# Kernel optimization log

Measured on AMD Instinct MI355X. Metric: run time of the kernel, lower is better.

Reference implementation:

```python
import jax, jax.numpy as jnp
import numpy as np
import math

B, N, DIM, H, DH, NNULL = 2, 2048, 1024, 16, 64, 2
SCALE = 8.0
LN_EPS = 1e-5


def _alibi_slopes(heads):
    # heads is a power of 2 here (16): slopes = start * start**i
    start = 2.0 ** (-(2.0 ** (-(math.log2(heads) - 3))))
    return np.array([start * (start ** i) for i in range(heads)], dtype=np.float32)


def setup_inputs() -> dict:
    key = jax.random.key(0)
    ks = jax.random.split(key, 6)
    inner = H * DH
    return {
        "x": jax.random.normal(ks[0], (B, N, DIM), dtype=jnp.float32),
        "norm_g": jnp.ones((DIM,), jnp.float32),
        "norm_b": jnp.zeros((DIM,), jnp.float32),
        "Wq": jax.random.normal(ks[1], (DIM, inner), jnp.float32) * 0.02,
        "Wkv": jax.random.normal(ks[2], (DIM, 2 * inner), jnp.float32) * 0.02,
        "q_scale": jnp.ones((DH,), jnp.float32),
        "k_scale": jnp.ones((DH,), jnp.float32),
        "null_kv": jax.random.normal(ks[3], (H, 2 * NNULL, DH), jnp.float32),
        "Wout": jax.random.normal(ks[4], (inner, DIM), jnp.float32) * 0.02,
    }


def _l2norm(t):
    # matches F.normalize: x / max(||x||, 1e-12)
    n = jnp.sqrt(jnp.sum(t * t, axis=-1, keepdims=True))
    return t / jnp.maximum(n, 1e-12)


def reference(x, norm_g, norm_b, Wq, Wkv, q_scale, k_scale, null_kv, Wout):
    b, n, dim = x.shape
    h, dh, nn = H, DH, NNULL
    j = n + nn

    # NOTE: faithful to source -- K/V come from the PRE-norm x (kv_input bound
    # before x = self.norm(x)); only Q uses the LayerNorm'd x.
    mu = jnp.mean(x, axis=-1, keepdims=True)
    var = jnp.mean((x - mu) ** 2, axis=-1, keepdims=True)
    xn = (x - mu) * jax.lax.rsqrt(var + LN_EPS) * norm_g + norm_b

    q = (xn @ Wq).reshape(b, n, h, dh).transpose(0, 2, 1, 3)          # b h n d
    kv = x @ Wkv
    k, v = jnp.split(kv, 2, axis=-1)
    k = k.reshape(b, n, h, dh).transpose(0, 2, 1, 3)                   # b h n d
    v = v.reshape(b, n, h, dh).transpose(0, 2, 1, 3)

    # null kv: (h, 2*nn, dh) -> (h, nn, 2, dh)
    null = null_kv.reshape(h, nn, 2, dh)
    nk = jnp.broadcast_to(null[:, :, 0, :][None], (b, h, nn, dh))
    nv = jnp.broadcast_to(null[:, :, 1, :][None], (b, h, nn, dh))
    k = jnp.concatenate([nk, k], axis=2)                               # b h j d
    v = jnp.concatenate([nv, v], axis=2)

    q = _l2norm(q) * q_scale
    k = _l2norm(k) * k_scale

    sim = jnp.einsum('bhid,bhjd->bhij', q, k) * SCALE                  # b h n j

    # ALiBi bias: rows at positions j-n..j-1, cols 0..j-1
    irow = jnp.arange(j - n, j)
    jcol = jnp.arange(j)
    bias = -jnp.abs(jcol[None, :] - irow[:, None]).astype(sim.dtype)   # (n, j)
    slopes = jnp.asarray(_alibi_slopes(h))[:, None, None]              # (h,1,1)
    sim = sim + slopes * bias

    # causal mask: triu with offset j - n + 1 (null kv always visible)
    causal = jnp.triu(jnp.ones((n, j), dtype=bool), k=j - n + 1)
    neg = jnp.finfo(sim.dtype).max
    sim = jnp.where(causal[None, None], -neg, sim)

    attn = jax.nn.softmax(sim, axis=-1)
    out = jnp.einsum('bhij,bhjd->bhid', attn, v)
    out = out.transpose(0, 2, 1, 3).reshape(b, n, h * dh)
    return out @ Wout
```

## Files before the change

kernel.cpp:

```cpp
#include <hip/hip_runtime.h>
#include <stdint.h>

#define H_    16
#define N_    2048
#define DIM_  1024
#define DH_   64
#define NN_   2
#define J_    2050
#define JP_   2112
#define B_    2
#define M_    4096
#define NSEG_ 84

typedef unsigned short u16;
typedef unsigned int u32;
typedef short bf16x8 __attribute__((ext_vector_type(8)));
typedef float f32x4 __attribute__((ext_vector_type(4)));

__device__ __forceinline__ u16 f2b(float f) {
  union { float f; unsigned int i; } v; v.f = f;
  unsigned int r = v.i + 0x7fffu + ((v.i >> 16) & 1u);
  return (u16)(r >> 16);
}
__device__ __forceinline__ float b2f(u16 u) {
  union { unsigned int i; float f; } v; v.i = ((unsigned int)u) << 16; return v.f;
}
__device__ __forceinline__ float lo2f(u32 u) {
  union { u32 i; float f; } v; v.i = u << 16; return v.f;
}
__device__ __forceinline__ float hi2f(u32 u) {
  union { u32 i; float f; } v; v.i = u & 0xffff0000u; return v.f;
}
__device__ __forceinline__ void unp8(const uint4 u, float* d) {
  d[0] = lo2f(u.x); d[1] = hi2f(u.x); d[2] = lo2f(u.y); d[3] = hi2f(u.y);
  d[4] = lo2f(u.z); d[5] = hi2f(u.z); d[6] = lo2f(u.w); d[7] = hi2f(u.w);
}
__device__ __forceinline__ void dma16(const u16* g, u16* l) {
  __builtin_amdgcn_global_load_lds(
      (const __attribute__((address_space(1))) u32*)(const void*)g,
      (__attribute__((address_space(3))) u32*)(void*)l, 16, 0, 0);
}

__global__ __launch_bounds__(256) void ktranspose_cast(const float* __restrict__ in,
                                                       u16* __restrict__ out, int R, int C) {
  __shared__ float tile[32][33];
  int tx = threadIdx.x & 31, ty = threadIdx.x >> 5;
  int c0 = blockIdx.x * 32, r0 = blockIdx.y * 32;
  #pragma unroll
  for (int i = 0; i < 32; i += 8)
    tile[ty + i][tx] = in[(size_t)(r0 + ty + i) * C + c0 + tx];
  __syncthreads();
  #pragma unroll
  for (int i = 0; i < 32; i += 8)
    out[(size_t)(c0 + ty + i) * R + r0 + tx] = f2b(tile[tx][ty + i]);
}

__global__ __launch_bounds__(256) void lnorm_k(const float* __restrict__ x,
                                               const float* __restrict__ g,
                                               const float* __restrict__ bb,
                                               u16* __restrict__ xn,
                                               u16* __restrict__ xbf) {
  int row = blockIdx.x;
  int t = threadIdx.x;
  float4 rw = *(const float4*)(x + (size_t)row * DIM_ + t * 4);
  float v0 = rw.x, v1 = rw.y, v2 = rw.z, v3 = rw.w;
  uint2 cw;
  cw.x = (unsigned)f2b(v0) | ((unsigned)f2b(v1) << 16);
  cw.y = (unsigned)f2b(v2) | ((unsigned)f2b(v3) << 16);
  *(uint2*)(xbf + (size_t)row * DIM_ + t * 4) = cw;
  float s = v0 + v1 + v2 + v3;
  float ss = v0 * v0 + v1 * v1 + v2 * v2 + v3 * v3;
  #pragma unroll
  for (int o = 32; o; o >>= 1) { s += __shfl_xor(s, o, 64); ss += __shfl_xor(ss, o, 64); }
  __shared__ float red[8];
  int lane = t & 63, w = t >> 6;
  if (lane == 0) { red[w] = s; red[4 + w] = ss; }
  __syncthreads();
  float S = red[0] + red[1] + red[2] + red[3];
  float SS = red[4] + red[5] + red[6] + red[7];
  float mu = S * (1.0f / DIM_);
  float var = SS * (1.0f / DIM_) - mu * mu;
  float rs = rsqrtf(var + 1e-5f);
  float4 gv = *(const float4*)(g + t * 4);
  float4 bv = *(const float4*)(bb + t * 4);
  uint2 ow;
  ow.x = (unsigned)f2b((v0 - mu) * rs * gv.x + bv.x) |
         ((unsigned)f2b((v1 - mu) * rs * gv.y + bv.y) << 16);
  ow.y = (unsigned)f2b((v2 - mu) * rs * gv.z + bv.z) |
         ((unsigned)f2b((v3 - mu) * rs * gv.w + bv.w) << 16);
  *(uint2*)(xn + (size_t)row * DIM_ + t * 4) = ow;
}

template <int MODE>
__global__ __launch_bounds__(256, 4) void gemm_k(const u16* __restrict__ A,
                                                 const u16* __restrict__ BT,
                                                 void* __restrict__ dst0,
                                                 void* __restrict__ dst1,
                                                 const float* __restrict__ scale,
                                                 int M, int Nc, int K) {
  __shared__ u16 As[128 * 32];
  __shared__ u16 Bs[64 * 32];
  int tid = threadIdx.x, wv = tid >> 6, lane = tid & 63;
  int fm = lane & 15, fg = lane >> 4;
  int row0 = blockIdx.y * 128, col0 = blockIdx.x * 64;
  f32x4 acc[2][4] = {};
  int lr = lane >> 2, lc8 = (lane & 3) * 8;
  const u16* Ag = A + (size_t)(row0 + wv * 32 + lr) * K + lc8;
  const u16* Bg = BT + (size_t)(col0 + wv * 16 + lr) * K + lc8;
  u16* AsW = As + wv * 1024;
  u16* BsW = Bs + wv * 512;
  for (int k0 = 0; k0 < K; k0 += 32) {
    __syncthreads();
    dma16(Ag + k0, AsW);
    dma16(Ag + (size_t)16 * K + k0, AsW + 512);
    dma16(Bg + k0, BsW);
    __syncthreads();
    bf16x8 af0 = *(const bf16x8*)&As[(wv * 32 + fm) * 32 + fg * 8];
    bf16x8 af1 = *(const bf16x8*)&As[(wv * 32 + 16 + fm) * 32 + fg * 8];
    #pragma unroll
    for (int nt = 0; nt < 4; nt++) {
      bf16x8 bfr = *(const bf16x8*)&Bs[(nt * 16 + fm) * 32 + fg * 8];
      acc[0][nt] = __builtin_amdgcn_mfma_f32_16x16x32_bf16(af0, bfr, acc[0][nt], 0, 0, 0);
      acc[1][nt] = __builtin_amdgcn_mfma_f32_16x16x32_bf16(af1, bfr, acc[1][nt], 0, 0, 0);
    }
  }
  if (MODE == 1) {
    float* C = (float*)dst0;
    #pragma unroll
    for (int mt = 0; mt < 2; mt++)
      #pragma unroll
      for (int nt = 0; nt < 4; nt++)
        #pragma unroll
        for (int r = 0; r < 4; r++) {
          int m = row0 + wv * 32 + mt * 16 + fg * 4 + r;
          C[(size_t)m * Nc + col0 + nt * 16 + fm] = acc[mt][nt][r];
        }
  } else {
    bool isK = (MODE == 2) || (col0 < 1024);
    int h = ((MODE == 2) ? col0 : (isK ? col0 : col0 - 1024)) >> 6;
    float sv[4];
    if (isK) {
      #pragma unroll
      for (int nt = 0; nt < 4; nt++) sv[nt] = scale[nt * 16 + fm];
    }
    u16* Do = (u16*)((MODE == 3 && !isK) ? dst1 : dst0);
    #pragma unroll
    for (int mt = 0; mt < 2; mt++) {
      #pragma unroll
      for (int r = 0; r < 4; r++) {
        float inv = 1.0f;
        if (isK) {
          float ssp = 0.0f;
          #pragma unroll
          for (int nt = 0; nt < 4; nt++) ssp += acc[mt][nt][r] * acc[mt][nt][r];
          #pragma unroll
          for (int o = 1; o <= 8; o <<= 1) ssp += __shfl_xor(ssp, o, 64);
          inv = 1.0f / fmaxf(sqrtf(ssp), 1e-12f);
        }
        int m = row0 + wv * 32 + mt * 16 + fg * 4 + r;
        int b = m >> 11, n = m & 2047;
        size_t base;
        if (MODE == 2)      base = (((size_t)(b * H_ + h)) * N_ + n) * 64;
        else if (isK)       base = (((size_t)(b * H_ + h)) * JP_ + (n + NN_)) * 64;
        else                base = (((size_t)(b * H_ + h)) * J_ + (n + NN_)) * 64;
        #pragma unroll
        for (int nt = 0; nt < 4; nt++) {
          float val = acc[mt][nt][r];
          if (isK) val = val * inv * sv[nt];
          Do[base + nt * 16 + fm] = f2b(val);
        }
      }
    }
  }
}

__global__ __launch_bounds__(256) void vtransp_k(const u16* __restrict__ Vb,
                                                 const float* __restrict__ nkv,
                                                 const float* __restrict__ ks,
                                                 u16* __restrict__ Kb,
                                                 u16* __restrict__ VTp) {
  __shared__ u16 tile[64][80];
  int t = threadIdx.x;
  int c = blockIdx.x, bh = blockIdx.y, h = bh & 15;
  int jl = t >> 2, dc = (t & 3) * 16;
  int j = c * 64 + jl;
  if (j < NN_) {
    float kvv[16];
    float kssp = 0.0f;
    #pragma unroll
    for (int e = 0; e < 16; e++) {
      float vv = nkv[(size_t)(h * 4 + 2 * j + 1) * 64 + dc + e];
      tile[jl][dc + e] = f2b(vv);
      float kv = nkv[(size_t)(h * 4 + 2 * j) * 64 + dc + e];
      kvv[e] = kv; kssp += kv * kv;
    }
    kssp += __shfl_xor(kssp, 1, 64);
    kssp += __shfl_xor(kssp, 2, 64);
    float inv = 1.0f / fmaxf(sqrtf(kssp), 1e-12f);
    #pragma unroll
    for (int e = 0; e < 16; e++)
      Kb[((size_t)bh * JP_ + j) * 64 + dc + e] = f2b(kvv[e] * inv * ks[dc + e]);
  } else if (j < J_) {
    const uint4* src = (const uint4*)(Vb + ((size_t)bh * J_ + j) * 64 + dc);
    *(uint4*)&tile[jl][dc] = src[0];
    *(uint4*)&tile[jl][dc + 8] = src[1];
  } else {
    uint4 z = {0, 0, 0, 0};
    *(uint4*)&tile[jl][dc] = z;
    *(uint4*)&tile[jl][dc + 8] = z;
  }
  __syncthreads();
  int d = t >> 2, p0 = (t & 3) * 16;
  u16 tmp[16] __attribute__((aligned(16)));
  #pragma unroll
  for (int e = 0; e < 16; e++) {
    int pos = p0 + e;
    int h2 = pos >> 5, rem = pos & 31;
    int fgp = rem >> 3, tt = rem & 7;
    int nt = tt >> 2, r = tt & 3;
    int jloc = (h2 * 2 + nt) * 16 + fgp * 4 + r;
    tmp[e] = tile[jloc][d];
  }
  uint4* dstp = (uint4*)(VTp + ((size_t)bh * 64 + d) * JP_ + c * 64 + p0);
  dstp[0] = ((uint4*)tmp)[0];
  dstp[1] = ((uint4*)tmp)[1];
}

__global__ __launch_bounds__(256, 6) void attn_k(const u16* __restrict__ Qn,
                                                 const u16* __restrict__ Kb,
                                                 const u16* __restrict__ VTp,
                                                 const float* __restrict__ qs,
                                                 const float* __restrict__ ks,
                                                 u16* __restrict__ partials) {
  __shared__ u16 Ks0[64 * 32], Ks1[64 * 32];
  __shared__ u16 Vs0[64 * 32], Vs1[64 * 32];
  int tid = threadIdx.x;
  int wv = tid >> 6, lane = tid & 63;
  int fm = lane & 15, fg = lane >> 4;
  int bh = blockIdx.y, h = bh & 15;
  int cum = 0, qt = 0, seg = 0;
  #pragma unroll 1
  for (int i = 0; i < 32; i++) {
    int t = 31 - i, s = (t + 9) >> 3;
    if ((int)blockIdx.x < cum + s) { qt = t; seg = (int)blockIdx.x - cum; break; }
    cum += s;
  }
  int q0 = qt * 64;
  int q = q0 + wv * 16 + fm;
  float slope = exp2f(-0.5f * (float)(h + 1));
  float prod = fabsf(qs[lane] * ks[lane]);
  #pragma unroll
  for (int o = 32; o; o >>= 1) prod = fmaxf(prod, __shfl_xor(prod, o, 64));
  float Mb = 8.0f * prod;
  const u16* qp = Qn + ((size_t)bh * N_ + q) * 64 + fg * 8;
  bf16x8 qf0 = *(const bf16x8*)(qp);
  bf16x8 qf1 = *(const bf16x8*)(qp + 32);
  f32x4 accO[4] = {};
  float lp = 0.0f;
  int lr = lane >> 2, lc8 = (lane & 3) * 8;
  const u16* KbBH = Kb + (size_t)bh * JP_ * 64;
  const u16* VTbh = VTp + (size_t)bh * 64 * JP_;
  int c0 = seg * 8;
  int c1 = min(c0 + 8, qt + 2);
  for (int c = c0; c < c1; c++) {
    int jb = c * 64;
    __syncthreads();
    const u16* Kg = KbBH + (size_t)jb * 64 + (size_t)(wv * 16 + lr) * 64 + lc8;
    dma16(Kg,      Ks0 + wv * 512);
    dma16(Kg + 32, Ks1 + wv * 512);
    const u16* Vg = VTbh + (size_t)(wv * 16 + lr) * JP_ + jb + lc8;
    dma16(Vg,      Vs0 + wv * 512);
    dma16(Vg + 32, Vs1 + wv * 512);
    __syncthreads();
    f32x4 accS[4] = {};
    #pragma unroll
    for (int nt = 0; nt < 4; nt++) {
      bf16x8 kf0 = *(const bf16x8*)&Ks0[(nt * 16 + fm) * 32 + fg * 8];
      accS[nt] = __builtin_amdgcn_mfma_f32_16x16x32_bf16(kf0, qf0, accS[nt], 0, 0, 0);
      bf16x8 kf1 = *(const bf16x8*)&Ks1[(nt * 16 + fm) * 32 + fg * 8];
      accS[nt] = __builtin_amdgcn_mfma_f32_16x16x32_bf16(kf1, qf1, accS[nt], 0, 0, 0);
    }
    union { bf16x8 v; u16 s[8]; } P0, P1;
    #pragma unroll
    for (int nt = 0; nt < 4; nt++) {
      #pragma unroll
      for (int r = 0; r < 4; r++) {
        int jj = jb + nt * 16 + fg * 4 + r;
        float arg = fmaf(accS[nt][r], 8.0f, slope * (float)(jj - q - 2)) - Mb;
        float p = (jj <= q + 2) ? __expf(arg) : 0.0f;
        u16 pb = f2b(p);
        lp += b2f(pb);
        if (nt < 2) P0.s[nt * 4 + r] = pb;
        else        P1.s[(nt - 2) * 4 + r] = pb;
      }
    }
    #pragma unroll
    for (int nt = 0; nt < 4; nt++) {
      bf16x8 vf0 = *(const bf16x8*)&Vs0[(nt * 16 + fm) * 32 + fg * 8];
      accO[nt] = __builtin_amdgcn_mfma_f32_16x16x32_bf16(vf0, P0.v, accO[nt], 0, 0, 0);
      bf16x8 vf1 = *(const bf16x8*)&Vs1[(nt * 16 + fm) * 32 + fg * 8];
      accO[nt] = __builtin_amdgcn_mfma_f32_16x16x32_bf16(vf1, P1.v, accO[nt], 0, 0, 0);
    }
  }
  lp += __shfl_xor(lp, 16, 64);
  lp += __shfl_xor(lp, 32, 64);
  u16* P = partials + ((size_t)bh * NSEG_ + blockIdx.x) * 4224;
  int sq = wv * 16 + fm;
  #pragma unroll
  for (int nt = 0; nt < 4; nt++) {
    uint2 ow;
    ow.x = (unsigned)f2b(accO[nt][0]) | ((unsigned)f2b(accO[nt][1]) << 16);
    ow.y = (unsigned)f2b(accO[nt][2]) | ((unsigned)f2b(accO[nt][3]) << 16);
    *(uint2*)(P + sq * 64 + nt * 16 + fg * 4) = ow;
  }
  if (fg == 0) *(float*)(P + 4096 + 2 * sq) = lp;
}

__global__ __launch_bounds__(256) void comb_k(const u16* __restrict__ partials,
                                              u16* __restrict__ AO) {
  int qt = blockIdx.x, bh = blockIdx.y, b = bh >> 4, h = bh & 15;
  int t = threadIdx.x, q = t >> 2, dq = (t & 3) * 16;
  int s = (qt + 9) >> 3;
  int cum = 0;
  for (int tt = qt + 1; tt < 32; tt++) cum += (tt + 9) >> 3;
  float acc[16] = {};
  float lsum = 0.0f;
  for (int k = 0; k < s; k++) {
    const u16* P = partials + ((size_t)bh * NSEG_ + cum + k) * 4224;
    uint4 a = *(const uint4*)(P + q * 64 + dq);
    uint4 bq = *(const uint4*)(P + q * 64 + dq + 8);
    float tmp[8];
    unp8(a, tmp);
    #pragma unroll
    for (int e = 0; e < 8; e++) acc[e] += tmp[e];
    unp8(bq, tmp);
    #pragma unroll
    for (int e = 0; e < 8; e++) acc[8 + e] += tmp[e];
    lsum += *(const float*)(P + 4096 + 2 * q);
  }
  float linv = 1.0f / lsum;
  int n = qt * 64 + q;
  u16* dst = AO + (((size_t)(b * N_ + n)) * H_ + h) * 64 + dq;
  u16 ov[16] __attribute__((aligned(16)));
  #pragma unroll
  for (int e = 0; e < 16; e++) ov[e] = f2b(acc[e] * linv);
  *(uint4*)dst = ((uint4*)ov)[0];
  *(uint4*)(dst + 8) = ((uint4*)ov)[1];
}

extern "C" void kernel_launch(void* const* d_in, const int* in_sizes, int n_in,
                              void* d_out, int out_size, void* d_ws, size_t ws_size,
                              hipStream_t stream) {
  const float* x    = (const float*)d_in[0];
  const float* ng   = (const float*)d_in[1];
  const float* nb   = (const float*)d_in[2];
  const float* Wq   = (const float*)d_in[3];
  const float* Wkv  = (const float*)d_in[4];
  const float* qs   = (const float*)d_in[5];
  const float* ks   = (const float*)d_in[6];
  const float* nkv  = (const float*)d_in[7];
  const float* Wout = (const float*)d_in[8];
  float* out = (float*)d_out;
  char* ws = (char*)d_ws;

  u16* xn    = (u16*)(ws + 0);
  u16* WoutT = (u16*)(ws + 8388608);
  u16* Qn    = (u16*)(ws + 10485760);
  u16* Kb    = (u16*)(ws + 18874368);
  u16* VTp   = (u16*)(ws + 27525120);
  u16* xbf   = (u16*)(ws + 36175872);
  u16* WqT   = (u16*)(ws + 44564480);
  u16* WkvT  = (u16*)(ws + 46661632);
  u16* Vb    = (u16*)(ws + 50855936);
  u16* parts = xbf;
  u16* AO    = xn;

  hipMemsetAsync(Kb, 0, 8650752, stream);
  ktranspose_cast<<<dim3(32, 32), 256, 0, stream>>>(Wq, WqT, 1024, 1024);
  ktranspose_cast<<<dim3(64, 32), 256, 0, stream>>>(Wkv, WkvT, 1024, 2048);
  ktranspose_cast<<<dim3(32, 32), 256, 0, stream>>>(Wout, WoutT, 1024, 1024);
  lnorm_k<<<4096, 256, 0, stream>>>(x, ng, nb, xn, xbf);
  gemm_k<2><<<dim3(16, 32), 256, 0, stream>>>(xn, WqT, Qn, nullptr, qs, M_, 1024, 1024);
  gemm_k<3><<<dim3(32, 32), 256, 0, stream>>>(xbf, WkvT, Kb, Vb, ks, M_, 2048, 1024);
  vtransp_k<<<dim3(33, 32), 256, 0, stream>>>(Vb, nkv, ks, Kb, VTp);
  attn_k<<<dim3(NSEG_, 32), 256, 0, stream>>>(Qn, Kb, VTp, qs, ks, parts);
  comb_k<<<dim3(32, 32), 256, 0, stream>>>(parts, AO);
  gemm_k<1><<<dim3(16, 32), 256, 0, stream>>>(AO, WoutT, out, nullptr, nullptr, M_, 1024, 1024);
}
```

Before: 238.8 us.

## Swizzle LDS layouts, deepen GEMM K-tile to 64, use packed bf16 conversion

The GEMM now stages a 64-wide K slice per iteration (twice the LDS tile) with an XOR swizzle on the LDS column blocks, halving the number of barrier pairs and reducing LDS bank conflicts on fragment reads. The attention kernel applies a similar XOR swizzle to the K/V tiles loaded by global_load_lds. Float-to-bf16 packing switches to the HIP packed conversion intrinsic. The larger tiles raise LDS use and drop the occupancy hint of 4 blocks per CU, which may lower occupancy.

```diff
diff --git a/kernel.cpp b/kernel.cpp
--- a/kernel.cpp
+++ b/kernel.cpp
@@ -1,4 +1,5 @@
 #include <hip/hip_runtime.h>
+#include <hip/hip_bf16.h>
 #include <stdint.h>
 
 #define H_    16
@@ -35,6 +36,11 @@
   d[0] = lo2f(u.x); d[1] = hi2f(u.x); d[2] = lo2f(u.y); d[3] = hi2f(u.y);
   d[4] = lo2f(u.z); d[5] = hi2f(u.z); d[6] = lo2f(u.w); d[7] = hi2f(u.w);
 }
+__device__ __forceinline__ u32 pk2(float a, float b) {
+  union { __hip_bfloat162 h; u32 u; } x;
+  x.h = __float22bfloat162_rn(make_float2(a, b));
+  return x.u;
+}
 __device__ __forceinline__ void dma16(const u16* g, u16* l) {
   __builtin_amdgcn_global_load_lds(
       (const __attribute__((address_space(1))) u32*)(const void*)g,
@@ -65,8 +71,8 @@
   float4 rw = *(const float4*)(x + (size_t)row * DIM_ + t * 4);
   float v0 = rw.x, v1 = rw.y, v2 = rw.z, v3 = rw.w;
   uint2 cw;
-  cw.x = (unsigned)f2b(v0) | ((unsigned)f2b(v1) << 16);
-  cw.y = (unsigned)f2b(v2) | ((unsigned)f2b(v3) << 16);
+  cw.x = pk2(v0, v1);
+  cw.y = pk2(v2, v3);
   *(uint2*)(xbf + (size_t)row * DIM_ + t * 4) = cw;
   float s = v0 + v1 + v2 + v3;
   float ss = v0 * v0 + v1 * v1 + v2 * v2 + v3 * v3;
@@ -84,60 +90,77 @@
   float4 gv = *(const float4*)(g + t * 4);
   float4 bv = *(const float4*)(bb + t * 4);
   uint2 ow;
-  ow.x = (unsigned)f2b((v0 - mu) * rs * gv.x + bv.x) |
-         ((unsigned)f2b((v1 - mu) * rs * gv.y + bv.y) << 16);
-  ow.y = (unsigned)f2b((v2 - mu) * rs * gv.z + bv.z) |
-         ((unsigned)f2b((v3 - mu) * rs * gv.w + bv.w) << 16);
+  ow.x = pk2((v0 - mu) * rs * gv.x + bv.x, (v1 - mu) * rs * gv.y + bv.y);
+  ow.y = pk2((v2 - mu) * rs * gv.z + bv.z, (v3 - mu) * rs * gv.w + bv.w);
   *(uint2*)(xn + (size_t)row * DIM_ + t * 4) = ow;
 }
 
 template <int MODE>
-__global__ __launch_bounds__(256, 4) void gemm_k(const u16* __restrict__ A,
-                                                 const u16* __restrict__ BT,
-                                                 void* __restrict__ dst0,
-                                                 void* __restrict__ dst1,
-                                                 const float* __restrict__ scale,
-                                                 int M, int Nc, int K) {
-  __shared__ u16 As[128 * 32];
-  __shared__ u16 Bs[64 * 32];
+__global__ __launch_bounds__(256) void gemm_k(const u16* __restrict__ A,
+                                              const u16* __restrict__ BT,
+                                              void* __restrict__ dst0,
+                                              void* __restrict__ dst1,
+                                              const float* __restrict__ scale,
+                                              int M, int Nc, int K) {
+  __shared__ u16 As[128 * 64];
+  __shared__ u16 Bs[64 * 64];
   int tid = threadIdx.x, wv = tid >> 6, lane = tid & 63;
   int fm = lane & 15, fg = lane >> 4;
   int row0 = blockIdx.y * 128, col0 = blockIdx.x * 64;
   f32x4 acc[2][4] = {};
-  int lr = lane >> 2, lc8 = (lane & 3) * 8;
-  const u16* Ag = A + (size_t)(row0 + wv * 32 + lr) * K + lc8;
-  const u16* Bg = BT + (size_t)(col0 + wv * 16 + lr) * K + lc8;
-  u16* AsW = As + wv * 1024;
-  u16* BsW = Bs + wv * 512;
-  for (int k0 = 0; k0 < K; k0 += 32) {
+  int srow = lane >> 3;
+  int skb = ((lane & 7) ^ srow) * 8;
+  const u16* Ag = A + (size_t)(row0 + wv * 32 + srow) * K + skb;
+  const u16* Bg = BT + (size_t)(col0 + wv * 16 + srow) * K + skb;
+  u16* AsW = As + (wv * 32) * 64;
+  u16* BsW = Bs + (wv * 16) * 64;
+  int fr7 = fm & 7;
+  int ak0 = (fg ^ fr7) * 8;
+  int ak1 = ((fg + 4) ^ fr7) * 8;
+  for (int k0 = 0; k0 < K; k0 += 64) {
     __syncthreads();
-    dma16(Ag + k0, AsW);
-    dma16(Ag + (size_t)16 * K + k0, AsW + 512);
-    dma16(Bg + k0, BsW);
+    dma16(Ag + k0,                    AsW);
+    dma16(Ag + (size_t)8 * K + k0,    AsW + 8 * 64);
+    dma16(Ag + (size_t)16 * K + k0,   AsW + 16 * 64);
+    dma16(Ag + (size_t)24 * K + k0,   AsW + 24 * 64);
+    dma16(Bg + k0,                    BsW);
+    dma16(Bg + (size_t)8 * K + k0,    BsW + 8 * 64);
     __syncthreads();
-    bf16x8 af0 = *(const bf16x8*)&As[(wv * 32 + fm) * 32 + fg * 8];
-    bf16x8 af1 = *(const bf16x8*)&As[(wv * 32 + 16 + fm) * 32 + fg * 8];
+    bf16x8 af0[2], af1[2], bf0[4], bf1[4];
+    #pragma unroll
+    for (int mt = 0; mt < 2; mt++) {
+      int rbase = (wv * 32 + mt * 16 + fm) * 64;
+      af0[mt] = *(const bf16x8*)&As[rbase + ak0];
+      af1[mt] = *(const bf16x8*)&As[rbase + ak1];
+    }
     #pragma unroll
     for (int nt = 0; nt < 4; nt++) {
-      bf16x8 bfr = *(const bf16x8*)&Bs[(nt * 16 + fm) * 32 + fg * 8];
-      acc[0][nt] = __builtin_amdgcn_mfma_f32_16x16x32_bf16(af0, bfr, acc[0][nt], 0, 0, 0);
-      acc[1][nt] = __builtin_amdgcn_mfma_f32_16x16x32_bf16(af1, bfr, acc[1][nt], 0, 0, 0);
-    }
+      int rbase = (nt * 16 + fm) * 64;
+      bf0[nt] = *(const bf16x8*)&Bs[rbase + ak0];
+      bf1[nt] = *(const bf16x8*)&Bs[rbase + ak1];
+    }
+    #pragma unroll
+    for (int mt = 0; mt < 2; mt++)
+      #pragma unroll
+      for (int nt = 0; nt < 4; nt++) {
+        acc[mt][nt] = __builtin_amdgcn_mfma_f32_16x16x32_bf16(af0[mt], bf0[nt], acc[mt][nt], 0, 0, 0);
+        acc[mt][nt] = __builtin_amdgcn_mfma_f32_16x16x32_bf16(af1[mt], bf1[nt], acc[mt][nt], 0, 0, 0);
+      }
   }
   if (MODE == 1) {
     float* C = (float*)dst0;
     #pragma unroll
     for (int mt = 0; mt < 2; mt++)
       #pragma unroll
-      for (int nt = 0; nt < 4; nt++)
+      for (int r = 0; r < 4; r++) {
+        int m = row0 + wv * 32 + mt * 16 + fg * 4 + r;
         #pragma unroll
-        for (int r = 0; r < 4; r++) {
-          int m = row0 + wv * 32 + mt * 16 + fg * 4 + r;
+        for (int nt = 0; nt < 4; nt++)
           C[(size_t)m * Nc + col0 + nt * 16 + fm] = acc[mt][nt][r];
-        }
+      }
   } else {
     bool isK = (MODE == 2) || (col0 < 1024);
-    int h = ((MODE == 2) ? col0 : (isK ? col0 : col0 - 1024)) >> 6;
+    int h = (isK ? col0 : col0 - 1024) >> 6;
     float sv[4];
     if (isK) {
       #pragma unroll
@@ -257,7 +280,9 @@
   bf16x8 qf1 = *(const bf16x8*)(qp + 32);
   f32x4 accO[4] = {};
   float lp = 0.0f;
-  int lr = lane >> 2, lc8 = (lane & 3) * 8;
+  int lr = lane >> 2;
+  int kbs = ((lane & 3) ^ ((lane >> 3) & 3)) * 8;
+  int fs = (fg ^ ((fm >> 1) & 3)) * 8;
   const u16* KbBH = Kb + (size_t)bh * JP_ * 64;
   const u16* VTbh = VTp + (size_t)bh * 64 * JP_;
   int c0 = seg * 8;
@@ -265,19 +290,19 @@
   for (int c = c0; c < c1; c++) {
     int jb = c * 64;
     __syncthreads();
-    const u16* Kg = KbBH + (size_t)jb * 64 + (size_t)(wv * 16 + lr) * 64 + lc8;
+    const u16* Kg = KbBH + (size_t)(jb + wv * 16 + lr) * 64 + kbs;
     dma16(Kg,      Ks0 + wv * 512);
     dma16(Kg + 32, Ks1 + wv * 512);
-    const u16* Vg = VTbh + (size_t)(wv * 16 + lr) * JP_ + jb + lc8;
+    const u16* Vg = VTbh + (size_t)(wv * 16 + lr) * JP_ + jb + kbs;
     dma16(Vg,      Vs0 + wv * 512);
     dma16(Vg + 32, Vs1 + wv * 512);
     __syncthreads();
     f32x4 accS[4] = {};
     #pragma unroll
     for (int nt = 0; nt < 4; nt++) {
-      bf16x8 kf0 = *(const bf16x8*)&Ks0[(nt * 16 + fm) * 32 + fg * 8];
+      bf16x8 kf0 = *(const bf16x8*)&Ks0[(nt * 16 + fm) * 32 + fs];
       accS[nt] = __builtin_amdgcn_mfma_f32_16x16x32_bf16(kf0, qf0, accS[nt], 0, 0, 0);
-      bf16x8 kf1 = *(const bf16x8*)&Ks1[(nt * 16 + fm) * 32 + fg * 8];
+      bf16x8 kf1 = *(const bf16x8*)&Ks1[(nt * 16 + fm) * 32 + fs];
       accS[nt] = __builtin_amdgcn_mfma_f32_16x16x32_bf16(kf1, qf1, accS[nt], 0, 0, 0);
     }
     union { bf16x8 v; u16 s[8]; } P0, P1;
@@ -296,9 +321,9 @@
     }
     #pragma unroll
     for (int nt = 0; nt < 4; nt++) {
-      bf16x8 vf0 = *(const bf16x8*)&Vs0[(nt * 16 + fm) * 32 + fg * 8];
+      bf16x8 vf0 = *(const bf16x8*)&Vs0[(nt * 16 + fm) * 32 + fs];
       accO[nt] = __builtin_amdgcn_mfma_f32_16x16x32_bf16(vf0, P0.v, accO[nt], 0, 0, 0);
-      bf16x8 vf1 = *(const bf16x8*)&Vs1[(nt * 16 + fm) * 32 + fg * 8];
+      bf16x8 vf1 = *(const bf16x8*)&Vs1[(nt * 16 + fm) * 32 + fs];
       accO[nt] = __builtin_amdgcn_mfma_f32_16x16x32_bf16(vf1, P1.v, accO[nt], 0, 0, 0);
     }
   }
@@ -309,8 +334,8 @@
   #pragma unroll
   for (int nt = 0; nt < 4; nt++) {
     uint2 ow;
-    ow.x = (unsigned)f2b(accO[nt][0]) | ((unsigned)f2b(accO[nt][1]) << 16);
-    ow.y = (unsigned)f2b(accO[nt][2]) | ((unsigned)f2b(accO[nt][3]) << 16);
+    ow.x = pk2(accO[nt][0], accO[nt][1]);
+    ow.y = pk2(accO[nt][2], accO[nt][3]);
     *(uint2*)(P + sq * 64 + nt * 16 + fg * 4) = ow;
   }
   if (fg == 0) *(float*)(P + 4096 + 2 * sq) = lp;
```

After: 231.3 us. 3.2% less time.
